# Kernel optimization log

Measured on AMD Instinct MI355X. Metric: run time of the kernel, lower is better.

## Reference

```python
import jax, jax.numpy as jnp
import numpy as np

N_NODES = 50000
N_EDGES = 800000
DIM = 128
N_LAYERS = 4
EPS = 1e-5  # BatchNorm1d default eps


def setup_inputs() -> dict:
    key = jax.random.key(0)
    k_x, k_e, k_w = jax.random.split(key, 3)
    x = jax.random.normal(k_x, (N_NODES, DIM), dtype=jnp.float32)
    edge_index = jax.random.randint(k_e, (2, N_EDGES), 0, N_NODES, dtype=jnp.int32)
    # stacked per-layer params (input_dim == hidden_dim == DIM)
    Ws = jax.random.normal(k_w, (N_LAYERS, DIM, DIM), dtype=jnp.float32) * (1.0 / np.sqrt(DIM))
    bs = jnp.zeros((N_LAYERS, DIM), jnp.float32)
    gammas = jnp.ones((N_LAYERS, DIM), jnp.float32)
    betas = jnp.zeros((N_LAYERS, DIM), jnp.float32)
    return {"x": x, "edge_index": edge_index, "Ws": Ws, "bs": bs,
            "gammas": gammas, "betas": betas}


def gcn_conv(x, W, b, src, dst, n):
    # PyG GCNConv: h = X W; out = D^{-1/2}(A+I)D^{-1/2} h + b
    h = x @ W                                       # [N, D]
    deg = jnp.zeros((n,), h.dtype).at[dst].add(1.0) + 1.0  # +1 self-loop
    dis = jax.lax.rsqrt(deg)                        # deg > 0 due to self-loops
    msg = h[src] * (dis[src] * dis[dst])[:, None]   # [E, D] gather + scale
    out = jnp.zeros_like(h).at[dst].add(msg)        # scatter-add aggregate
    out = out + h * (dis * dis)[:, None]            # self-loop term, norm = 1/deg
    return out + b


def batchnorm(z, gamma, beta):
    # BatchNorm1d training-mode math: batch mean, biased variance
    mu = z.mean(axis=0)
    var = z.var(axis=0)
    return (z - mu) * jax.lax.rsqrt(var + EPS) * gamma + beta


def reference(x, edge_index, Ws, bs, gammas, betas):
    src, dst = edge_index[0], edge_index[1]
    z = x
    for i in range(N_LAYERS):
        z = gcn_conv(z, Ws[i], bs[i], src, dst, z.shape[0])
        z = jax.nn.relu(z)
        z = batchnorm(z, gammas[i], betas[i])
        # Dropout: identity (eval mode / deterministic reference)
    return z
```

## Files before the change

### kernel.cpp

```cpp
#include <hip/hip_runtime.h>

#define N_NODES 50000
#define N_EDGES 800000
#define DIM 128
#define NLAYERS 4
#define BN_EPS 1e-5f
#define SCAN_BLOCKS 196
#define WS2 72

typedef __attribute__((ext_vector_type(8))) short short8;
typedef __attribute__((ext_vector_type(4))) float f32x4;

__device__ __forceinline__ float bf2f(unsigned short u){
    union { unsigned int i; float f; } x; x.i = ((unsigned int)u) << 16; return x.f;
}
__device__ __forceinline__ unsigned short f2bf(float f){
    union { float f; unsigned int i; } x; x.f = f;
    unsigned int lsb = (x.i >> 16) & 1u;
    unsigned int r = x.i + 0x7fffu + lsb;
    return (unsigned short)(r >> 16);
}

struct P4 { int2 a, b, c, d; };

__device__ __forceinline__ P4 loadP_mask(const int2* __restrict__ ep, int base,
                                         int sub, int lim){
    P4 p;
    int i0 = base + sub, i1 = base + 4 + sub, i2 = base + 8 + sub, i3 = base + 12 + sub;
    p.a = (i0 < lim) ? ep[i0] : make_int2(0, 0);
    p.b = (i1 < lim) ? ep[i1] : make_int2(0, 0);
    p.c = (i2 < lim) ? ep[i2] : make_int2(0, 0);
    p.d = (i3 < lim) ? ep[i3] : make_int2(0, 0);
    return p;
}
__device__ __forceinline__ P4 loadP_full(const int2* __restrict__ ep, int base,
                                         int sub){
    P4 p;
    p.a = ep[base + sub];
    p.b = ep[base + 4 + sub];
    p.c = ep[base + 8 + sub];
    p.d = ep[base + 12 + sub];
    return p;
}
__device__ __forceinline__ P4 loadP(const int2* __restrict__ ep, int base,
                                    int sub, int lim){
    if (lim - base >= 16) return loadP_full(ep, base, sub);
    return loadP_mask(ep, base, sub, lim);
}


__global__ __launch_bounds__(256) void k_zero(int* __restrict__ p, int n){
    int i = blockIdx.x * 256 + threadIdx.x;
    if (i < n) p[i] = 0;
}

__global__ __launch_bounds__(256) void k_count(const int* __restrict__ dst,
                                               int* __restrict__ degcnt){
    int e = blockIdx.x * 256 + threadIdx.x;
    if (e < N_EDGES) atomicAdd(&degcnt[dst[e]], 1);
}

__global__ __launch_bounds__(256) void k_scan1(const int* __restrict__ degcnt,
                                               int* __restrict__ rowptr,
                                               int* __restrict__ bsum,
                                               float* __restrict__ dis){
    __shared__ int tmp[256];
    int t = threadIdx.x;
    int i = blockIdx.x * 256 + t;
    int v = (i < N_NODES) ? degcnt[i] : 0;
    if (i < N_NODES) dis[i] = rsqrtf((float)v + 1.0f);
    tmp[t] = v;
    __syncthreads();
    #pragma unroll
    for (int off = 1; off < 256; off <<= 1){
        int u = (t >= off) ? tmp[t - off] : 0;
        __syncthreads();
        tmp[t] += u;
        __syncthreads();
    }
    if (i < N_NODES) rowptr[i] = tmp[t] - v;
    if (t == 255) bsum[blockIdx.x] = tmp[255];
}

__global__ __launch_bounds__(256) void k_scan3(const int* __restrict__ bsum,
                                               int* __restrict__ rowptr,
                                               int* __restrict__ wptr){
    __shared__ int tmp[256];
    int t = threadIdx.x;
    int v = (t < SCAN_BLOCKS) ? bsum[t] : 0;
    tmp[t] = v;
    __syncthreads();
    #pragma unroll
    for (int off = 1; off < 256; off <<= 1){
        int u = (t >= off) ? tmp[t - off] : 0;
        __syncthreads();
        tmp[t] += u;
        __syncthreads();
    }
    int boff = (blockIdx.x == 0) ? 0 : tmp[blockIdx.x - 1];
    int i = blockIdx.x * 256 + t;
    if (i < N_NODES){
        int r = rowptr[i] + boff;
        rowptr[i] = r; wptr[i] = r;
    }
    if (i == 0) rowptr[N_NODES] = N_EDGES;
}

__global__ __launch_bounds__(256) void k_fill(const int* __restrict__ src,
                                              const int* __restrict__ dst,
                                              const float* __restrict__ dis,
                                              int* __restrict__ wptr,
                                              int2* __restrict__ epair){
    int e = blockIdx.x * 256 + threadIdx.x;
    if (e < N_EDGES){
        int s = src[e], d = dst[e];
        float w = dis[s] * dis[d];
        int p = atomicAdd(&wptr[d], 1);
        int2 pr; pr.x = s; pr.y = __float_as_int(w);
        epair[p] = pr;
    }
}


template<int MODE>
__global__ __launch_bounds__(256) void k_gemm(const void* __restrict__ zraw,
                                              const float* __restrict__ W,
                                              const float* __restrict__ stats,
                                              const float* __restrict__ gamma,
                                              const float* __restrict__ beta,
                                              unsigned short* __restrict__ hb){
    __shared__ short whi[DIM * WS2];
    __shared__ short wlo[DIM * WS2];
    __shared__ float scs[DIM], shs[DIM];
    __shared__ float part[256];
    __shared__ float b2[DIM];
    int tid = threadIdx.x;

    if (MODE == 1){
        if (tid < DIM){
            float mu  = stats[tid] * (1.0f / N_NODES);
            float var = stats[DIM + tid] * (1.0f / N_NODES) - mu * mu;
            float sc  = rsqrtf(var + BN_EPS) * gamma[tid];
            scs[tid] = sc;
            shs[tid] = beta[tid] - mu * sc;
        }
        __syncthreads();
        {
            int c = tid >> 1, half = tid & 1;
            float acc = 0.f;
            int k0 = half * 64;
            #pragma unroll 4
            for (int k = k0; k < k0 + 64; k++)
                acc = fmaf(shs[k], W[k*DIM + c], acc);
            part[tid] = acc;
        }
    } else {
        if (tid < DIM) b2[tid] = 0.f;
    }

    int lane = tid & 63;
    int wv   = tid >> 6;
    int m = lane & 15;
    int q = lane >> 4;
    int row0 = blockIdx.x * 64 + wv * 16;
    int arow = row0 + m;
    bool avalid = arow < N_NODES;

    f32x4 acc[8];
    #pragma unroll
    for (int t = 0; t < 8; t++) acc[t] = (f32x4){0.f, 0.f, 0.f, 0.f};

    #pragma unroll
    for (int half = 0; half < 2; half++){
        #pragma unroll
        for (int it = 0; it < 4; it++){
            int ch = tid + 256*it;
            int kc = ch >> 7, c = ch & 127;
            int kbase = half*64 + kc*8;
            short8 vh, vl;
            #pragma unroll
            for (int i = 0; i < 8; i++){
                float v = W[(kbase + i)*DIM + c];
                if (MODE == 1) v *= scs[kbase + i];
                unsigned short h = f2bf(v);
                float lo = v - bf2f(h);
                vh[i] = (short)h;
                vl[i] = (short)f2bf(lo);
            }
            *(short8*)&whi[c*WS2 + kc*8] = vh;
            *(short8*)&wlo[c*WS2 + kc*8] = vl;
        }
        __syncthreads();
        if (MODE == 1 && half == 0){
            if (tid < DIM) b2[tid] = part[2*tid] + part[2*tid + 1];
        }

        #pragma unroll
        for (int gl2 = 0; gl2 < 2; gl2++){
            int gg = half*2 + gl2;
            short8 a = {0,0,0,0,0,0,0,0};
            if (avalid){
                if (MODE == 0){
                    const float* xp = (const float*)zraw + (size_t)arow*DIM + gg*32 + q*8;
                    float4 v0 = *(const float4*)xp;
                    float4 v1 = *(const float4*)(xp + 4);
                    a[0] = (short)f2bf(v0.x); a[1] = (short)f2bf(v0.y);
                    a[2] = (short)f2bf(v0.z); a[3] = (short)f2bf(v0.w);
                    a[4] = (short)f2bf(v1.x); a[5] = (short)f2bf(v1.y);
                    a[6] = (short)f2bf(v1.z); a[7] = (short)f2bf(v1.w);
                } else {
                    a = *(const short8*)((const unsigned short*)zraw
                          + (size_t)gg*N_NODES*32 + (size_t)arow*32 + q*8);
                }
            }
            #pragma unroll
            for (int t = 0; t < 8; t++){
                int col = t*16 + m;
                int off = col*WS2 + gl2*32 + q*8;
                short8 bh = *(const short8*)&whi[off];
                short8 bl = *(const short8*)&wlo[off];
                acc[t] = __builtin_amdgcn_mfma_f32_16x16x32_bf16(a, bh, acc[t], 0, 0, 0);
                acc[t] = __builtin_amdgcn_mfma_f32_16x16x32_bf16(a, bl, acc[t], 0, 0, 0);
            }
        }
        if (half == 0) __syncthreads();
    }

    #pragma unroll
    for (int t = 0; t < 8; t++){
        int colg = t*16 + m;
        float bz = b2[colg];
        size_t base = (size_t)(t >> 1)*N_NODES*32 + (t & 1)*16 + m;
        #pragma unroll
        for (int r = 0; r < 4; r++){
            int row = row0 + q*4 + r;
            if (row < N_NODES)
                hb[base + (size_t)row*32] = f2bf(acc[t][r] + bz);
        }
    }
}

__global__ __launch_bounds__(256) void k_agg(const unsigned short* __restrict__ h,
                                             const int* __restrict__ rowptr,
                                             const int2* __restrict__ epair,
                                             const float* __restrict__ dis,
                                             const float* __restrict__ bias,
                                             unsigned short* __restrict__ out,
                                             float* __restrict__ stats){
    int lane = threadIdx.x & 63;
    int w    = threadIdx.x >> 6;
    int g    = blockIdx.x & 3;
    int sub  = lane >> 4;
    int cp   = lane & 15;
    const ushort2* hg = (const ushort2*)(h + (size_t)g * N_NODES * 32);
    ushort2* og = (ushort2*)(out + (size_t)g * N_NODES * 32);
    float b0 = bias[g*32 + 2*cp], b1 = bias[g*32 + 2*cp + 1];
    float s0 = 0.f, s1 = 0.f, q0 = 0.f, q1 = 0.f;
    int bg = blockIdx.x >> 2;
    int nstride = (gridDim.x >> 2) * 4;

    int node = bg*4 + w;
    int ne0 = 0, ne1 = 0;
    ushort2 nhv; nhv.x = 0; nhv.y = 0;
    float ndi = 0.f;
    P4 nP = {{0,0},{0,0},{0,0},{0,0}};
    if (node < N_NODES){
        ne0 = rowptr[node];
        ne1 = rowptr[node + 1];
        nhv = hg[node*16 + cp];
        ndi = dis[node];
        nP  = loadP(epair, ne0, sub, ne1);
    }

    while (node < N_NODES){
        int e0 = ne0, e1 = ne1;
        ushort2 hv = nhv;
        float di = ndi;
        P4 P = nP;

        int nnext = node + nstride;
        if (nnext < N_NODES){
            ne0 = rowptr[nnext];
            ne1 = rowptr[nnext + 1];
            nhv = hg[nnext*16 + cp];
            ndi = dis[nnext];
        } else { ne0 = 0; ne1 = 0; }

        float pa0 = 0.f, pa1 = 0.f, pb0 = 0.f, pb1 = 0.f;
        float pc0 = 0.f, pc1 = 0.f, pd0 = 0.f, pd1 = 0.f;
        if (sub == 0){
            float dii = di * di;
            pa0 = bf2f(hv.x) * dii; pa1 = bf2f(hv.y) * dii;
        }

        int e = e0;
        while (e < e1){
            int en = e + 16;
            P4 Pn = {{0,0},{0,0},{0,0},{0,0}};
            if (en < e1) Pn = loadP(epair, en, sub, e1);
            ushort2 X0 = hg[P.a.x*16 + cp];
            ushort2 X1 = hg[P.b.x*16 + cp];
            ushort2 X2 = hg[P.c.x*16 + cp];
            ushort2 X3 = hg[P.d.x*16 + cp];
            float w0 = __int_as_float(P.a.y), w1 = __int_as_float(P.b.y);
            float w2 = __int_as_float(P.c.y), w3 = __int_as_float(P.d.y);
            pa0 = fmaf(bf2f(X0.x), w0, pa0); pa1 = fmaf(bf2f(X0.y), w0, pa1);
            pb0 = fmaf(bf2f(X1.x), w1, pb0); pb1 = fmaf(bf2f(X1.y), w1, pb1);
            pc0 = fmaf(bf2f(X2.x), w2, pc0); pc1 = fmaf(bf2f(X2.y), w2, pc1);
            pd0 = fmaf(bf2f(X3.x), w3, pd0); pd1 = fmaf(bf2f(X3.y), w3, pd1);
            P = Pn;
            e = en;
        }

        float r0 = (pa0 + pb0) + (pc0 + pd0);
        float r1 = (pa1 + pb1) + (pc1 + pd1);
        r0 += __shfl_xor(r0, 16); r1 += __shfl_xor(r1, 16);
        r0 += __shfl_xor(r0, 32); r1 += __shfl_xor(r1, 32);
        if (sub == 0){
            float a0 = fmaxf(r0 + b0, 0.f);
            float a1 = fmaxf(r1 + b1, 0.f);
            ushort2 ov; ov.x = f2bf(a0); ov.y = f2bf(a1);
            og[node*16 + cp] = ov;
            s0 += a0; s1 += a1; q0 += a0*a0; q1 += a1*a1;
        }

        if (nnext < N_NODES)
            nP = loadP(epair, ne0, sub, ne1);
        node = nnext;
    }

    __shared__ float red[4][16][4];
    if (sub == 0){
        red[w][cp][0] = s0; red[w][cp][1] = s1;
        red[w][cp][2] = q0; red[w][cp][3] = q1;
    }
    __syncthreads();
    if (w == 0 && sub == 0){
        #pragma unroll
        for (int ww = 1; ww < 4; ww++){
            s0 += red[ww][cp][0]; s1 += red[ww][cp][1];
            q0 += red[ww][cp][2]; q1 += red[ww][cp][3];
        }
        int c = g*32 + 2*cp;
        atomicAdd(&stats[c],         s0);
        atomicAdd(&stats[c + 1],     s1);
        atomicAdd(&stats[DIM + c],     q0);
        atomicAdd(&stats[DIM + c + 1], q1);
    }
}

__global__ __launch_bounds__(256) void k_bn(const uint4* __restrict__ in,
                                            const float* __restrict__ stats,
                                            const float* __restrict__ gamma,
                                            const float* __restrict__ beta,
                                            float4* __restrict__ outf){
    __shared__ float scs[DIM], shs[DIM];
    int tid = threadIdx.x;
    if (tid < DIM){
        float mu  = stats[tid] * (1.0f / N_NODES);
        float var = stats[DIM + tid] * (1.0f / N_NODES) - mu * mu;
        float sc  = rsqrtf(var + BN_EPS) * gamma[tid];
        scs[tid] = sc;
        shs[tid] = beta[tid] - mu * sc;
    }
    __syncthreads();

    int i = blockIdx.x * 256 + tid;
    if (i >= N_NODES * DIM / 8) return;
    int row = i >> 4;
    int c = (i * 8) & (DIM - 1);
    int gg = c >> 5, wi = c & 31;
    uint4 raw = in[gg*(N_NODES*4) + row*4 + (wi >> 3)];
    unsigned int u[4] = {raw.x, raw.y, raw.z, raw.w};
    float v[8];
    #pragma unroll
    for (int j = 0; j < 4; j++){
        v[2*j]   = bf2f((unsigned short)(u[j] & 0xffff));
        v[2*j+1] = bf2f((unsigned short)(u[j] >> 16));
    }
    float4 r0, r1;
    r0.x = fmaf(v[0], scs[c+0], shs[c+0]);
    r0.y = fmaf(v[1], scs[c+1], shs[c+1]);
    r0.z = fmaf(v[2], scs[c+2], shs[c+2]);
    r0.w = fmaf(v[3], scs[c+3], shs[c+3]);
    r1.x = fmaf(v[4], scs[c+4], shs[c+4]);
    r1.y = fmaf(v[5], scs[c+5], shs[c+5]);
    r1.z = fmaf(v[6], scs[c+6], shs[c+6]);
    r1.w = fmaf(v[7], scs[c+7], shs[c+7]);
    outf[2*i]   = r0;
    outf[2*i+1] = r1;
}


extern "C" void kernel_launch(void* const* d_in, const int* in_sizes, int n_in,
                              void* d_out, int out_size, void* d_ws, size_t ws_size,
                              hipStream_t stream){
    const float* x   = (const float*)d_in[0];
    const int*   src = (const int*)d_in[1];
    const int*   dst = src + N_EDGES;
    const float* Ws  = (const float*)d_in[2];
    const float* bs  = (const float*)d_in[3];
    const float* gs  = (const float*)d_in[4];
    const float* be  = (const float*)d_in[5];

    char* w = (char*)d_ws;
    int*   degcnt = (int*)(w);
    float* stats  = (float*)(w + 200000);
    float* dis    = (float*)(w + 208192);
    int*   rowptr = (int*)(w + 408192);
    int*   wptr   = (int*)(w + 608208);
    int*   bsum   = (int*)(w + 808208);
    int2*  epair  = (int2*)(w + 875280);
    unsigned short* bufA = (unsigned short*)(w + 7275280);
    unsigned short* hb   = (unsigned short*)(w + 20075280);

    k_zero<<<(51024 + 255)/256, 256, 0, stream>>>(degcnt, 51024);
    k_count<<<3125, 256, 0, stream>>>(dst, degcnt);
    k_scan1<<<SCAN_BLOCKS, 256, 0, stream>>>(degcnt, rowptr, bsum, dis);
    k_scan3<<<SCAN_BLOCKS, 256, 0, stream>>>(bsum, rowptr, wptr);
    k_fill<<<3125, 256, 0, stream>>>(src, dst, dis, wptr, epair);

    for (int L = 0; L < NLAYERS; L++){
        const float* Wl = Ws + L*DIM*DIM;
        if (L == 0)
            k_gemm<0><<<(N_NODES + 63)/64, 256, 0, stream>>>(x, Wl,
                    nullptr, nullptr, nullptr, hb);
        else
            k_gemm<1><<<(N_NODES + 63)/64, 256, 0, stream>>>(bufA, Wl,
                    stats + (L-1)*256, gs + (L-1)*DIM, be + (L-1)*DIM, hb);
        k_agg<<<2048, 256, 0, stream>>>(hb, rowptr, epair, dis, bs + L*DIM,
                                        bufA, stats + L*256);
    }
    k_bn<<<3125, 256, 0, stream>>>((const uint4*)bufA, stats + 3*256,
                                   gs + 3*DIM, be + 3*DIM, (float4*)d_out);
}
```

Baseline: 550.8 us.

## Map feature groups to XCD pairs and use nontemporal edge loads and output stores

Block IDs in the aggregation kernel are remapped so that each 32-column feature group lands on a pair of XCDs, assuming round-robin dispatch of blocks across the eight XCDs. This keeps each group's h slice resident in fewer L2 caches. Edge-pair loads and the aggregated output stores become nontemporal so that streaming data does not evict the reused h rows. The risks are that the XCD dispatch assumption may not hold, and that the grid size must be a multiple of eight for the node-stride mapping to cover every node correctly.

```diff
diff --git a/kernel.cpp b/kernel.cpp
--- a/kernel.cpp
+++ b/kernel.cpp
@@ -21,25 +21,33 @@
     return (unsigned short)(r >> 16);
 }
 
+__device__ __forceinline__ int2 ldnt2(const int2* __restrict__ p){
+    long long v = __builtin_nontemporal_load((const long long*)p);
+    int2 r;
+    r.x = (int)(unsigned int)(v & 0xffffffffLL);
+    r.y = (int)(unsigned int)(((unsigned long long)v) >> 32);
+    return r;
+}
+
 struct P4 { int2 a, b, c, d; };
 
 __device__ __forceinline__ P4 loadP_mask(const int2* __restrict__ ep, int base,
                                          int sub, int lim){
     P4 p;
     int i0 = base + sub, i1 = base + 4 + sub, i2 = base + 8 + sub, i3 = base + 12 + sub;
-    p.a = (i0 < lim) ? ep[i0] : make_int2(0, 0);
-    p.b = (i1 < lim) ? ep[i1] : make_int2(0, 0);
-    p.c = (i2 < lim) ? ep[i2] : make_int2(0, 0);
-    p.d = (i3 < lim) ? ep[i3] : make_int2(0, 0);
+    p.a = (i0 < lim) ? ldnt2(ep + i0) : make_int2(0, 0);
+    p.b = (i1 < lim) ? ldnt2(ep + i1) : make_int2(0, 0);
+    p.c = (i2 < lim) ? ldnt2(ep + i2) : make_int2(0, 0);
+    p.d = (i3 < lim) ? ldnt2(ep + i3) : make_int2(0, 0);
     return p;
 }
 __device__ __forceinline__ P4 loadP_full(const int2* __restrict__ ep, int base,
                                          int sub){
     P4 p;
-    p.a = ep[base + sub];
-    p.b = ep[base + 4 + sub];
-    p.c = ep[base + 8 + sub];
-    p.d = ep[base + 12 + sub];
+    p.a = ldnt2(ep + base + sub);
+    p.b = ldnt2(ep + base + 4 + sub);
+    p.c = ldnt2(ep + base + 8 + sub);
+    p.d = ldnt2(ep + base + 12 + sub);
     return p;
 }
 __device__ __forceinline__ P4 loadP(const int2* __restrict__ ep, int base,
@@ -249,14 +257,15 @@
                                              float* __restrict__ stats){
     int lane = threadIdx.x & 63;
     int w    = threadIdx.x >> 6;
-    int g    = blockIdx.x & 3;
+    int xcd  = blockIdx.x & 7;
+    int g    = xcd >> 1;
+    int bg   = (blockIdx.x >> 3) * 2 + (xcd & 1);
     int sub  = lane >> 4;
     int cp   = lane & 15;
     const ushort2* hg = (const ushort2*)(h + (size_t)g * N_NODES * 32);
     ushort2* og = (ushort2*)(out + (size_t)g * N_NODES * 32);
     float b0 = bias[g*32 + 2*cp], b1 = bias[g*32 + 2*cp + 1];
     float s0 = 0.f, s1 = 0.f, q0 = 0.f, q1 = 0.f;
-    int bg = blockIdx.x >> 2;
     int nstride = (gridDim.x >> 2) * 4;
 
     int node = bg*4 + w;
@@ -320,7 +329,8 @@
             float a0 = fmaxf(r0 + b0, 0.f);
             float a1 = fmaxf(r1 + b1, 0.f);
             ushort2 ov; ov.x = f2bf(a0); ov.y = f2bf(a1);
-            og[node*16 + cp] = ov;
+            union { ushort2 u2; unsigned int u; } cv; cv.u2 = ov;
+            __builtin_nontemporal_store(cv.u, (unsigned int*)&og[node*16 + cp]);
             s0 += a0; s1 += a1; q0 += a0*a0; q1 += a1*a1;
         }
 
```

Result: slower. 613.0 us (+11.3%).
